# Optimization experiments

Measured on AMD Instinct MI355X. Metric: run time of the kernel, lower is better.

Reference implementation:

```python
import jax, jax.numpy as jnp
import numpy as np
import math

S_DIM = 512
Z_DIM = 64
B, L = 64, 512
NUM_HEADS = 4
HEAD_DIM = S_DIM // NUM_HEADS
N_AA = 20


def _layer_norm(x, eps=1e-5):
    mu = jnp.mean(x, axis=-1, keepdims=True)
    var = jnp.var(x, axis=-1, keepdims=True)
    return (x - mu) * jax.lax.rsqrt(var + eps)


def setup_inputs() -> dict:
    key = jax.random.key(0)
    ks = jax.random.split(key, 16)
    scale = 0.02
    d = {
        's': jax.random.normal(ks[0], (B, L, S_DIM), jnp.float32),
        'z': jax.random.normal(ks[1], (B, L, Z_DIM), jnp.float32),
        'wq': jax.random.normal(ks[2], (S_DIM, S_DIM), jnp.float32) * scale,
        'bq': jnp.zeros((S_DIM,), jnp.float32),
        'wk': jax.random.normal(ks[3], (S_DIM, S_DIM), jnp.float32) * scale,
        'bk': jnp.zeros((S_DIM,), jnp.float32),
        'wv': jax.random.normal(ks[4], (S_DIM, S_DIM), jnp.float32) * scale,
        'bv': jnp.zeros((S_DIM,), jnp.float32),
        'wo': jax.random.normal(ks[5], (S_DIM, S_DIM), jnp.float32) * scale,
        'bo': jnp.zeros((S_DIM,), jnp.float32),
        'wp': jax.random.normal(ks[6], (S_DIM, N_AA), jnp.float32) * scale,
        'bp': jnp.zeros((N_AA,), jnp.float32),
        'pos_bias': jax.random.normal(ks[7], (512,), jnp.float32) * 0.3,
        'entropy_weight': jnp.ones((1,), jnp.float32) * 0.1,
        'ln_g': jnp.ones((S_DIM,), jnp.float32),
        'ln_b': jnp.zeros((S_DIM,), jnp.float32),
        'w1': jax.random.normal(ks[8], (S_DIM, 4 * S_DIM), jnp.float32) * scale,
        'b1': jnp.zeros((4 * S_DIM,), jnp.float32),
        'w2': jax.random.normal(ks[9], (4 * S_DIM, S_DIM), jnp.float32) * scale,
        'b2': jnp.zeros((S_DIM,), jnp.float32),
    }
    return d


def reference(s, z, wq, bq, wk, bk, wv, bv, wo, bo, wp, bp, pos_bias,
              entropy_weight, ln_g, ln_b, w1, b1, w2, b2):
    Bc, Lc, D = s.shape
    H, hd = NUM_HEADS, D // NUM_HEADS

    s_ln = _layer_norm(s)  # non-affine F.layer_norm

    # sequence-profile entropy
    logits = s_ln @ wp + bp                      # [B,L,20]
    profile_probs = jax.nn.softmax(logits, axis=-1)
    position_entropy = -jnp.sum(profile_probs * jnp.log(profile_probs + 1e-8), axis=-1)  # [B,L]

    q = (s_ln @ wq + bq).reshape(Bc, Lc, H, hd)
    k = (s_ln @ wk + bk).reshape(Bc, Lc, H, hd)
    v = (s_ln @ wv + bv).reshape(Bc, Lc, H, hd)

    scores = jnp.einsum('blhd,bmhd->bhlm', q, k) / math.sqrt(hd)  # [B,H,L,L]

    # bias injected only at query index 0, using batch-0 entropy (as in torch code)
    entropy_guidance = -position_entropy[0, :Lc] * entropy_weight[0]  # [L]
    total_bias = entropy_guidance + pos_bias[:Lc]                      # [L]
    scores = scores.at[:, :, 0, :].add(total_bias[None, None, :])

    attn_weights = jax.nn.softmax(scores, axis=-1)                     # [B,H,L,L]
    attn_out = jnp.einsum('bhlm,bmhd->blhd', attn_weights, v).reshape(Bc, Lc, D)

    s2 = s + (attn_out @ wo + bo)

    h = _layer_norm(s2) * ln_g + ln_b
    ffn_out = jax.nn.relu(h @ w1 + b1) @ w2 + b2
    s3 = s2 + ffn_out

    return (s3, z, attn_weights[:, 0, :, :], position_entropy, profile_probs)
```

## Files before the change

### kernel.cpp

```cpp
#include <hip/hip_runtime.h>
#include <hip/hip_bf16.h>
#include <math.h>

#define SDIM 512
#define BATCH 64
#define LSEQ 512
#define NHEAD 4
#define HDIM 128
#define NAA 20
#define NROWS (BATCH * LSEQ)
#define LDQKV 1536

typedef __attribute__((ext_vector_type(8))) short short8;
typedef __attribute__((ext_vector_type(4))) float f32x4;

__device__ __forceinline__ unsigned short f2bf(float f) {
    unsigned int x = __float_as_uint(f);
    unsigned int r = (x + 0x7fffu + ((x >> 16) & 1u)) >> 16;
    return (unsigned short)r;
}
__device__ __forceinline__ float bf2f(unsigned short u) {
    return __uint_as_float((unsigned int)u << 16);
}

__device__ __forceinline__ void load16_lds(const void* g, void* lds) {
    __builtin_amdgcn_global_load_lds(
        (const __attribute__((address_space(1))) unsigned int*)g,
        (__attribute__((address_space(3))) unsigned int*)lds, 16, 0, 0);
}

__device__ __forceinline__ void wtrans_dev(
    float (*tile)[33], const float* __restrict__ W,
    unsigned short* __restrict__ Wt, int K, int N, int bx, int by, int t)
{
    const int tx = t & 31, ty = t >> 5;
    const int n0 = bx * 32, k0 = by * 32;
    #pragma unroll
    for (int p = 0; p < 4; p++)
        tile[ty + p * 8][tx] = W[(size_t)(k0 + ty + p * 8) * N + n0 + tx];
    __syncthreads();
    #pragma unroll
    for (int p = 0; p < 4; p++)
        Wt[(size_t)(n0 + ty + p * 8) * K + k0 + tx] = f2bf(tile[tx][ty + p * 8]);
}

__global__ __launch_bounds__(256) void prep_kernel(
    const float* __restrict__ wq, const float* __restrict__ wk,
    const float* __restrict__ wv, const float* __restrict__ wo,
    const float* __restrict__ w1, const float* __restrict__ w2,
    const float* __restrict__ wp,
    const float* __restrict__ bq, const float* __restrict__ bk,
    const float* __restrict__ bv,
    const float* __restrict__ z,
    const float* __restrict__ s,
    unsigned short* __restrict__ wqkvt, unsigned short* __restrict__ wot,
    unsigned short* __restrict__ w1t, unsigned short* __restrict__ w2t,
    unsigned short* __restrict__ wpT,
    float* __restrict__ bqkv, float* __restrict__ zout,
    unsigned short* __restrict__ Xb)
{
    __shared__ float tile[32][33];
    const int id = blockIdx.x;
    const int t  = threadIdx.x;

    if (id < 256)  { wtrans_dev(tile, wq, wqkvt,          512,  512, id & 15,        id >> 4,        t); return; }
    if (id < 512)  { const int i = id - 256;  wtrans_dev(tile, wk, wqkvt + 262144, 512,  512, i & 15, i >> 4, t); return; }
    if (id < 768)  { const int i = id - 512;  wtrans_dev(tile, wv, wqkvt + 524288, 512,  512, i & 15, i >> 4, t); return; }
    if (id < 1024) { const int i = id - 768;  wtrans_dev(tile, wo, wot,            512,  512, i & 15, i >> 4, t); return; }
    if (id < 2048) { const int i = id - 1024; wtrans_dev(tile, w1, w1t,            512, 2048, i & 63, i >> 6, t); return; }
    if (id < 3072) { const int i = id - 2048; wtrans_dev(tile, w2, w2t,           2048,  512, i & 15, i >> 4, t); return; }
    if (id < 3136) {
        const int g = (id - 3072) * 256 + t;
        const int k = g & 511, j = g >> 9;
        float v = (j < NAA) ? wp[(size_t)k * NAA + j] : 0.0f;
        wpT[(size_t)j * 512 + k] = f2bf(v);
        return;
    }
    if (id == 3136) {
        bqkv[t]        = bq[t];       bqkv[t + 256]  = bq[t + 256];
        bqkv[512 + t]  = bk[t];       bqkv[768 + t]  = bk[t + 256];
        bqkv[1024 + t] = bv[t];       bqkv[1280 + t] = bv[t + 256];
        return;
    }
    if (id < 5185) {
        const size_t i = (size_t)(id - 3137) * 256 + t;
        ((float4*)zout)[i] = ((const float4*)z)[i];
        return;
    }
    {
        const int w = t >> 6, l = t & 63;
        const int r = (id - 5185) * 4 + w;
        const float* row = s + (size_t)r * SDIM;
        float4 a = *(const float4*)(row + l * 4);
        float4 b = *(const float4*)(row + 256 + l * 4);
        float x[8] = {a.x, a.y, a.z, a.w, b.x, b.y, b.z, b.w};

        float sum = 0.f, sq = 0.f;
        #pragma unroll
        for (int i = 0; i < 8; i++) { sum += x[i]; sq += x[i] * x[i]; }
        #pragma unroll
        for (int o = 1; o < 64; o <<= 1) {
            sum += __shfl_xor(sum, o);
            sq  += __shfl_xor(sq, o);
        }
        const float mean = sum * (1.0f / SDIM);
        const float var  = sq * (1.0f / SDIM) - mean * mean;
        const float inv  = rsqrtf(var + 1e-5f);

        float y[8];
        #pragma unroll
        for (int i = 0; i < 8; i++) y[i] = (x[i] - mean) * inv;

        unsigned short* orow = Xb + (size_t)r * SDIM;
        uint2 p0, p1;
        p0.x = (unsigned)f2bf(y[0]) | ((unsigned)f2bf(y[1]) << 16);
        p0.y = (unsigned)f2bf(y[2]) | ((unsigned)f2bf(y[3]) << 16);
        p1.x = (unsigned)f2bf(y[4]) | ((unsigned)f2bf(y[5]) << 16);
        p1.y = (unsigned)f2bf(y[6]) | ((unsigned)f2bf(y[7]) << 16);
        *(uint2*)(orow + l * 4)       = p0;
        *(uint2*)(orow + 256 + l * 4) = p1;
    }
}

template<int INMODE, bool AFFINE>
__global__ __launch_bounds__(256) void ln_kernel(
    const void* __restrict__ inp, unsigned short* __restrict__ out,
    const float* __restrict__ gamma, const float* __restrict__ beta)
{
    const int w = threadIdx.x >> 6, l = threadIdx.x & 63;
    const int r = blockIdx.x * 4 + w;

    float x[8];
    if (INMODE == 0) {
        const float* row = (const float*)inp + (size_t)r * SDIM;
        float4 a = *(const float4*)(row + l * 4);
        float4 b = *(const float4*)(row + 256 + l * 4);
        x[0] = a.x; x[1] = a.y; x[2] = a.z; x[3] = a.w;
        x[4] = b.x; x[5] = b.y; x[6] = b.z; x[7] = b.w;
    } else {
        const unsigned short* row = (const unsigned short*)inp + (size_t)r * SDIM;
        uint2 a = *(const uint2*)(row + l * 4);
        uint2 b = *(const uint2*)(row + 256 + l * 4);
        x[0] = bf2f((unsigned short)(a.x & 0xffff)); x[1] = bf2f((unsigned short)(a.x >> 16));
        x[2] = bf2f((unsigned short)(a.y & 0xffff)); x[3] = bf2f((unsigned short)(a.y >> 16));
        x[4] = bf2f((unsigned short)(b.x & 0xffff)); x[5] = bf2f((unsigned short)(b.x >> 16));
        x[6] = bf2f((unsigned short)(b.y & 0xffff)); x[7] = bf2f((unsigned short)(b.y >> 16));
    }

    float sum = 0.f, sq = 0.f;
    #pragma unroll
    for (int i = 0; i < 8; i++) { sum += x[i]; sq += x[i] * x[i]; }
    #pragma unroll
    for (int o = 1; o < 64; o <<= 1) {
        sum += __shfl_xor(sum, o);
        sq  += __shfl_xor(sq, o);
    }
    const float mean = sum * (1.0f / SDIM);
    const float var  = sq * (1.0f / SDIM) - mean * mean;
    const float inv  = rsqrtf(var + 1e-5f);

    float y[8];
    if (AFFINE) {
        float4 g0 = *(const float4*)(gamma + l * 4);
        float4 g1 = *(const float4*)(gamma + 256 + l * 4);
        float4 b0 = *(const float4*)(beta + l * 4);
        float4 b1 = *(const float4*)(beta + 256 + l * 4);
        y[0] = (x[0]-mean)*inv*g0.x + b0.x; y[1] = (x[1]-mean)*inv*g0.y + b0.y;
        y[2] = (x[2]-mean)*inv*g0.z + b0.z; y[3] = (x[3]-mean)*inv*g0.w + b0.w;
        y[4] = (x[4]-mean)*inv*g1.x + b1.x; y[5] = (x[5]-mean)*inv*g1.y + b1.y;
        y[6] = (x[6]-mean)*inv*g1.z + b1.z; y[7] = (x[7]-mean)*inv*g1.w + b1.w;
    } else {
        #pragma unroll
        for (int i = 0; i < 8; i++) y[i] = (x[i] - mean) * inv;
    }

    unsigned short* orow = out + (size_t)r * SDIM;
    uint2 p0, p1;
    p0.x = (unsigned)f2bf(y[0]) | ((unsigned)f2bf(y[1]) << 16);
    p0.y = (unsigned)f2bf(y[2]) | ((unsigned)f2bf(y[3]) << 16);
    p1.x = (unsigned)f2bf(y[4]) | ((unsigned)f2bf(y[5]) << 16);
    p1.y = (unsigned)f2bf(y[6]) | ((unsigned)f2bf(y[7]) << 16);
    *(uint2*)(orow + l * 4)       = p0;
    *(uint2*)(orow + 256 + l * 4) = p1;
}

__global__ __launch_bounds__(256) void profile_kernel(
    const unsigned short* __restrict__ A,
    const unsigned short* __restrict__ wpT,
    const float* __restrict__ bp,
    float* __restrict__ probs,
    float* __restrict__ pe)
{
    __shared__ __align__(16) unsigned short As[128 * 64];

    const int t = threadIdx.x;
    const int w = t >> 6, l = t & 63;
    const int lr = l & 15, lg = l >> 4;
    const int m0 = blockIdx.x * 128;

    f32x4 sacc[2][2];
    #pragma unroll
    for (int m = 0; m < 2; m++)
        #pragma unroll
        for (int n = 0; n < 2; n++)
            sacc[m][n] = (f32x4){0.f, 0.f, 0.f, 0.f};

    const int srow  = l >> 3;
    const int swz16 = ((l & 7) ^ srow) << 4;
    const char* pA[4];
    unsigned ldsoff[4];
    #pragma unroll
    for (int i = 0; i < 4; i++) {
        const int row = (w * 4 + i) * 8 + srow;
        pA[i] = (const char*)A + (size_t)(m0 + row) * 1024 + swz16;
        ldsoff[i] = (unsigned)(w * 4 + i) * 1024;
    }

    const int rsw   = (lr & 7) << 4;
    const int foff0 = (lg * 16) ^ rsw;
    const int foff1 = (64 + lg * 16) ^ rsw;
    int arow[2];
    #pragma unroll
    for (int m = 0; m < 2; m++) arow[m] = (w * 32 + m * 16 + lr) * 128;

    for (int k0 = 0; k0 < 512; k0 += 64) {
        const size_t kb = (size_t)k0 * 2;
        #pragma unroll
        for (int i = 0; i < 4; i++)
            load16_lds(pA[i] + kb, (char*)As + ldsoff[i]);
        __syncthreads();

        short8 af[2], bf[2];
        #pragma unroll
        for (int m = 0; m < 2; m++) af[m] = *(const short8*)((const char*)As + arow[m] + foff0);
        #pragma unroll
        for (int n = 0; n < 2; n++)
            bf[n] = *(const short8*)(wpT + (size_t)(n * 16 + lr) * 512 + k0 + lg * 8);
        #pragma unroll
        for (int m = 0; m < 2; m++)
            #pragma unroll
            for (int n = 0; n < 2; n++)
                sacc[m][n] = __builtin_amdgcn_mfma_f32_16x16x32_bf16(af[m], bf[n], sacc[m][n], 0, 0, 0);

        #pragma unroll
        for (int m = 0; m < 2; m++) af[m] = *(const short8*)((const char*)As + arow[m] + foff1);
        #pragma unroll
        for (int n = 0; n < 2; n++)
            bf[n] = *(const short8*)(wpT + (size_t)(n * 16 + lr) * 512 + k0 + 32 + lg * 8);
        #pragma unroll
        for (int m = 0; m < 2; m++)
            #pragma unroll
            for (int n = 0; n < 2; n++)
                sacc[m][n] = __builtin_amdgcn_mfma_f32_16x16x32_bf16(af[m], bf[n], sacc[m][n], 0, 0, 0);

        __syncthreads();
    }

    const float b0 = bp[lr];
    const float b1 = (lr < 4) ? bp[16 + lr] : 0.0f;
    #pragma unroll
    for (int m = 0; m < 2; m++) {
        #pragma unroll
        for (int j = 0; j < 4; j++) {
            const float v0 = sacc[m][0][j] + b0;
            const float e0 = __expf(v0);
            const float v1 = sacc[m][1][j] + b1;
            const float e1 = (lr < 4) ? __expf(v1) : 0.0f;
            float Sp = e0 + e1;
            float Tp = e0 * v0 + ((lr < 4) ? e1 * v1 : 0.0f);
            #pragma unroll
            for (int o = 1; o < 16; o <<= 1) {
                Sp += __shfl_xor(Sp, o);
                Tp += __shfl_xor(Tp, o);
            }
            const float inv = 1.0f / Sp;
            const int row = m0 + w * 32 + m * 16 + lg * 4 + j;
            probs[(size_t)row * NAA + lr] = e0 * inv;
            if (lr < 4) probs[(size_t)row * NAA + 16 + lr] = e1 * inv;
            if (lr == 0) pe[row] = logf(Sp) - Tp * inv;
        }
    }
}

template<int OMODE, bool BIAS, bool RELU, int RESID>
__global__ __launch_bounds__(512, 2) void mgemm7(
    const unsigned short* __restrict__ A, int lda,
    const unsigned short* __restrict__ Bt, int ldb,
    void* __restrict__ Cv, int ldc,
    const float* __restrict__ bias,
    const void* __restrict__ R, int ldr,
    int K)
{
    __shared__ __align__(16) char lds[131072];

    const int t = threadIdx.x;
    const int w = t >> 6, l = t & 63;
    const int wr = w >> 2, wc = w & 3;
    const int lg = l >> 4, lr = l & 15;

    const int gx   = gridDim.x;
    const int nwg  = gx * gridDim.y;
    const int flat = blockIdx.x + gx * blockIdx.y;
    const int cpx  = nwg >> 3;
    const int logical = (flat & 7) * cpx + (flat >> 3);
    const int m0 = (logical / gx) * 256, n0 = (logical % gx) * 256;

    f32x4 acc[8][4];
    #pragma unroll
    for (int m = 0; m < 8; m++)
        #pragma unroll
        for (int n = 0; n < 4; n++)
            acc[m][n] = (f32x4){0.f, 0.f, 0.f, 0.f};

    const int srow = t >> 3;
    const int sch  = (t & 7) ^ (srow & 7);

    auto stageA = [&](int kt, int d, int h) {
        const char* src = (const char*)A +
            ((size_t)(m0 + h * 128 + srow) * lda + sch * 8) * 2 + (size_t)kt * 128;
        char* dst = lds + d * 65536 + h * 16384 + t * 16;
        load16_lds(src, dst);
        load16_lds(src + (size_t)64 * lda * 2, dst + 8192);
    };
    auto stageB = [&](int kt, int d, int h) {
        const char* src = (const char*)Bt +
            ((size_t)(n0 + h * 128 + srow) * ldb + sch * 8) * 2 + (size_t)kt * 128;
        char* dst = lds + d * 65536 + 32768 + h * 16384 + t * 16;
        load16_lds(src, dst);
        load16_lds(src + (size_t)64 * ldb * 2, dst + 8192);
    };

    int aoff[4], boff[2], sw[2];
    #pragma unroll
    for (int mi = 0; mi < 4; mi++) aoff[mi] = (mi * 32 + wr * 16 + lr) * 128;
    #pragma unroll
    for (int ni = 0; ni < 2; ni++) boff[ni] = (ni * 64 + wc * 16 + lr) * 128;
    #pragma unroll
    for (int ks = 0; ks < 2; ks++) sw[ks] = ((ks * 4 + lg) ^ (lr & 7)) << 4;

    short8 afc[2][4];
    short8 bfc0[2][2];
    short8 bfc1[2][2];

    const int NI = K >> 7;

#define MPHASE(D, MH, NH, LOADA, LOADB, BAR, STAGE_STMT, WAIT_STMT) do {       \
    const char* Abase_ = lds + (D) * 65536 + (MH) * 16384;                     \
    const char* Bbase_ = lds + (D) * 65536 + 32768 + (NH) * 16384;             \
    if (LOADA) {                                                               \
        _Pragma("unroll")                                                      \
        for (int ks_ = 0; ks_ < 2; ks_++)                                      \
            _Pragma("unroll")                                                  \
            for (int mi_ = 0; mi_ < 4; mi_++)                                  \
                afc[ks_][mi_] = *(const short8*)(Abase_ + aoff[mi_] + sw[ks_]);\
    }                                                                          \
    short8 (&bf_)[2][2] = (NH) ? bfc1 : bfc0;                                  \
    if (LOADB) {                                                               \
        _Pragma("unroll")                                                      \
        for (int ks_ = 0; ks_ < 2; ks_++)                                      \
            _Pragma("unroll")                                                  \
            for (int ni_ = 0; ni_ < 2; ni_++)                                  \
                bf_[ks_][ni_] = *(const short8*)(Bbase_ + boff[ni_] + sw[ks_]);\
    }                                                                          \
    STAGE_STMT;                                                                \
    WAIT_STMT;                                                                 \
    if (BAR) {                                                                 \
        __builtin_amdgcn_s_barrier();                                          \
        asm volatile("s_waitcnt lgkmcnt(0)" ::: "memory");                     \
        __builtin_amdgcn_sched_barrier(0);                                     \
    }                                                                          \
    __builtin_amdgcn_s_setprio(1);                                             \
    _Pragma("unroll")                                                          \
    for (int ks_ = 0; ks_ < 2; ks_++)                                          \
        _Pragma("unroll")                                                      \
        for (int mi_ = 0; mi_ < 4; mi_++)                                      \
            _Pragma("unroll")                                                  \
            for (int ni_ = 0; ni_ < 2; ni_++)                                  \
                acc[(MH) * 4 + mi_][(NH) * 2 + ni_] =                          \
                    __builtin_amdgcn_mfma_f32_16x16x32_bf16(                   \
                        afc[ks_][mi_], bf_[ks_][ni_],                          \
                        acc[(MH) * 4 + mi_][(NH) * 2 + ni_], 0, 0, 0);         \
    __builtin_amdgcn_s_setprio(0);                                             \
    asm volatile("" ::: "memory");                                             \
} while (0)

    stageA(0, 0, 0); stageB(0, 0, 0); stageB(0, 0, 1); stageA(0, 0, 1);
    stageA(1, 1, 0); stageB(1, 1, 0);
    asm volatile("s_waitcnt vmcnt(4)" ::: "memory");
    __builtin_amdgcn_s_barrier();
    asm volatile("" ::: "memory");

    for (int it = 0; it < NI; ++it) {
        const bool more = (it + 1 < NI);
        const int T1 = 2 * it + 1, T2 = 2 * it + 2, T3 = 2 * it + 3;

        MPHASE(0, 0, 0, 1, 1, 1, { stageB(T1, 1, 1); }, {});
        MPHASE(0, 0, 1, 0, 1, 1, { stageA(T1, 1, 1); }, {});
        MPHASE(0, 1, 0, 1, 0, 1, { if (more) stageA(T2, 0, 0); }, {});
        MPHASE(0, 1, 1, 0, 0, 0, { if (more) stageB(T2, 0, 0); },
               { if (more) { asm volatile("s_waitcnt vmcnt(4)" ::: "memory"); }
                 else      { asm volatile("s_waitcnt vmcnt(0)" ::: "memory"); } });
        MPHASE(1, 0, 0, 1, 1, 1, { if (more) stageA(T2, 0, 1); }, {});
        MPHASE(1, 0, 1, 0, 1, 1, { if (more) stageB(T2, 0, 1); }, {});
        MPHASE(1, 1, 0, 1, 0, 1, { if (more) stageA(T3, 1, 0); }, {});
        MPHASE(1, 1, 1, 0, 0, 0, { if (more) stageB(T3, 1, 0); },
               { if (more) { asm volatile("s_waitcnt vmcnt(4)" ::: "memory"); } });
    }
#undef MPHASE

    __syncthreads();

    if (OMODE == 1) {
        unsigned short* cs = (unsigned short*)lds;
        #pragma unroll
        for (int nf = 0; nf < 4; nf++) {
            const int lcol = (nf >> 1) * 128 + (nf & 1) * 64 + wc * 16 + lr;
            const int col = n0 + lcol;
            const float bv = BIAS ? bias[col] : 0.0f;
            #pragma unroll
            for (int mf = 0; mf < 8; mf++) {
                const int lrow0 = (mf >> 2) * 128 + (mf & 3) * 32 + wr * 16 + lg * 4;
                #pragma unroll
                for (int j = 0; j < 4; j++) {
                    float v = acc[mf][nf][j] + bv;
                    if (RELU) v = fmaxf(v, 0.f);
                    const size_t grow = (size_t)(m0 + lrow0 + j);
                    if (RESID == 1) v += ((const float*)R)[grow * ldr + col];
                    if (RESID == 2) v += bf2f(((const unsigned short*)R)[grow * ldr + col]);
                    cs[(lrow0 + j) * 256 + lcol] = f2bf(v);
                }
            }
        }
        __syncthreads();
        unsigned short* Cp = (unsigned short*)Cv;
        #pragma unroll
        for (int i = 0; i < 16; i++) {
            const int slot = i * 512 + t;
            const int row = slot >> 5, c16 = slot & 31;
            short8 v = *(const short8*)(cs + row * 256 + c16 * 8);
            *(short8*)(Cp + (size_t)(m0 + row) * ldc + n0 + c16 * 8) = v;
        }
    } else {
        float* cf = (float*)lds;
        #pragma unroll
        for (int h = 0; h < 2; h++) {
            if (h) __syncthreads();
            #pragma unroll
            for (int nf = 0; nf < 4; nf++) {
                const int lcol = (nf >> 1) * 128 + (nf & 1) * 64 + wc * 16 + lr;
                const int col = n0 + lcol;
                const float bv = BIAS ? bias[col] : 0.0f;
                #pragma unroll
                for (int mi = 0; mi < 4; mi++) {
                    const int mf = h * 4 + mi;
                    const int lrow0 = (mf & 3) * 32 + wr * 16 + lg * 4;
                    #pragma unroll
                    for (int j = 0; j < 4; j++) {
                        float v = acc[mf][nf][j] + bv;
                        if (RELU) v = fmaxf(v, 0.f);
                        const size_t grow = (size_t)(m0 + h * 128 + lrow0 + j);
                        if (RESID == 1) v += ((const float*)R)[grow * ldr + col];
                        if (RESID == 2) v += bf2f(((const unsigned short*)R)[grow * ldr + col]);
                        cf[(lrow0 + j) * 256 + lcol] = v;
                    }
                }
            }
            __syncthreads();
            float* Cp = (float*)Cv;
            #pragma unroll
            for (int i = 0; i < 16; i++) {
                const int slot = i * 512 + t;
                const int row = slot >> 6, c4 = slot & 63;
                float4 v = *(const float4*)(cf + row * 256 + c4 * 4);
                *(float4*)(Cp + (size_t)(m0 + h * 128 + row) * ldc + n0 + c4 * 4) = v;
            }
        }
    }
}

__global__ __launch_bounds__(256, 2) void attn_mfma(
    const unsigned short* __restrict__ QKV,
    const float* __restrict__ pe,
    const float* __restrict__ ew,
    const float* __restrict__ pos,
    unsigned short* __restrict__ AOb,
    float* __restrict__ lgout)
{
    const int flat = blockIdx.x + 4 * (blockIdx.y + 4 * blockIdx.z);
    const int logical = ((flat & 7) << 7) + (flat >> 3);
    const int qt = logical & 3;
    const int h  = (logical >> 2) & 3;
    const int b  = logical >> 4;
    const int t  = threadIdx.x;
    const int w  = t >> 6, l = t & 63;
    const int lr = l & 15, lg = l >> 4;
    const int qbase = qt * 128 + w * 32;

    const unsigned short* Qp = QKV;
    const unsigned short* Kp = QKV + 512;
    const unsigned short* Vp = QKV + 1024;

    __shared__ __align__(16) unsigned short Ks[2][8192];
    __shared__ __align__(16) unsigned short Vt[8192];
    __shared__ __align__(16) unsigned short Pl[8192];
    __shared__ float tbs[512];

    {
        const float e0 = ew[0];
        tbs[t]       = -pe[t]       * e0 + pos[t];
        tbs[t + 256] = -pe[t + 256] * e0 + pos[t + 256];
    }

    short8 qf[2][4];
    #pragma unroll
    for (int fc = 0; fc < 2; fc++) {
        const size_t qrow = (size_t)(b * LSEQ + qbase + fc * 16 + lr) * LDQKV + h * HDIM;
        #pragma unroll
        for (int ks = 0; ks < 4; ks++)
            qf[fc][ks] = *(const short8*)(Qp + qrow + ks * 32 + lg * 8);
    }

    f32x4 oacc[2][8];
    #pragma unroll
    for (int m = 0; m < 2; m++)
        #pragma unroll
        for (int n = 0; n < 8; n++)
            oacc[m][n] = (f32x4){0.f, 0.f, 0.f, 0.f};
    float lpart[2] = {0.f, 0.f};

    const float scale = 0.08838834764831845f;
    unsigned short* Plw = Pl + w * 2048;

    auto stageK = [&](int kt, int buf) {
        #pragma unroll
        for (int it = 0; it < 4; it++) {
            const int bi = it * 4 + w;
            const int r  = bi * 4 + lg;
            const int sc = lr ^ (r & 7);
            const char* src = (const char*)Kp +
                (size_t)(b * LSEQ + kt * 64 + r) * (LDQKV * 2) + h * 256 + sc * 16;
            load16_lds(src, (char*)Ks[buf] + bi * 1024);
        }
    };
    const int k0v = (l & 31) * 2;
    const int d0v = w * 32 + (l >> 5) * 16;

    stageK(0, 0);
    short8 vc0, vc1, vc2, vc3, vn0, vn1, vn2, vn3;
    {
        const size_t vrow = (size_t)(b * LSEQ + k0v) * LDQKV + h * HDIM + d0v;
        vc0 = *(const short8*)(Vp + vrow);
        vc1 = *(const short8*)(Vp + vrow + 8);
        vc2 = *(const short8*)(Vp + vrow + LDQKV);
        vc3 = *(const short8*)(Vp + vrow + LDQKV + 8);
    }

    #pragma unroll 2
    for (int kt = 0; kt < 8; ++kt) {
        asm volatile("" ::: "memory");
        __builtin_amdgcn_s_barrier();
        asm volatile("" ::: "memory");

        if (kt < 7) {
            stageK(kt + 1, (kt + 1) & 1);
            const size_t vrow = (size_t)(b * LSEQ + (kt + 1) * 64 + k0v) * LDQKV + h * HDIM + d0v;
            vn0 = *(const short8*)(Vp + vrow);
            vn1 = *(const short8*)(Vp + vrow + 8);
            vn2 = *(const short8*)(Vp + vrow + LDQKV);
            vn3 = *(const short8*)(Vp + vrow + LDQKV + 8);
        }
        asm volatile("" ::: "memory");

        #pragma unroll
        for (int j = 0; j < 16; j++) {
            const int d = d0v + j;
            unsigned short lo = (unsigned short)((j < 8) ? vc0[j] : vc1[j - 8]);
            unsigned short hi = (unsigned short)((j < 8) ? vc2[j] : vc3[j - 8]);
            unsigned int pk = (unsigned)lo | ((unsigned)hi << 16);
            const int addr = d * 128 + ((((k0v >> 3) ^ (d & 7))) << 4) + (k0v & 7) * 2;
            *(unsigned int*)((char*)Vt + addr) = pk;
        }

        if (kt < 7) { asm volatile("s_waitcnt vmcnt(8)" ::: "memory"); }
        else        { asm volatile("s_waitcnt vmcnt(0)" ::: "memory"); }
        asm volatile("s_waitcnt lgkmcnt(0)" ::: "memory");
        __builtin_amdgcn_s_barrier();
        __builtin_amdgcn_sched_barrier(0);

        const unsigned short* Ksb = Ks[kt & 1];

        f32x4 sacc[4][2];
        #pragma unroll
        for (int fm = 0; fm < 4; fm++)
            #pragma unroll
            for (int fc = 0; fc < 2; fc++)
                sacc[fm][fc] = (f32x4){0.f, 0.f, 0.f, 0.f};
        #pragma unroll
        for (int ks = 0; ks < 4; ks++) {
            short8 af[4];
            #pragma unroll
            for (int fm = 0; fm < 4; fm++) {
                const int r2 = fm * 16 + lr;
                af[fm] = *(const short8*)((const char*)Ksb +
                          r2 * 256 + (((ks * 4 + lg) ^ (lr & 7)) << 4));
            }
            #pragma unroll
            for (int fm = 0; fm < 4; fm++)
                #pragma unroll
                for (int fc = 0; fc < 2; fc++)
                    sacc[fm][fc] = __builtin_amdgcn_mfma_f32_16x16x32_bf16(
                        af[fm], qf[fc][ks], sacc[fm][fc], 0, 0, 0);
        }

        #pragma unroll
        for (int fm = 0; fm < 4; fm++) {
            #pragma unroll
            for (int fc = 0; fc < 2; fc++) {
                float p0 = sacc[fm][fc][0] * scale;
                float p1 = sacc[fm][fc][1] * scale;
                float p2 = sacc[fm][fc][2] * scale;
                float p3 = sacc[fm][fc][3] * scale;
                if (qt == 0 && w == 0 && fc == 0 && lr == 0) {
                    const int kb = kt * 64 + fm * 16 + lg * 4;
                    p0 += tbs[kb + 0]; p1 += tbs[kb + 1];
                    p2 += tbs[kb + 2]; p3 += tbs[kb + 3];
                }
                p0 = __expf(p0); p1 = __expf(p1);
                p2 = __expf(p2); p3 = __expf(p3);
                lpart[fc] += (p0 + p1) + (p2 + p3);
                const int rq = fc * 16 + lr;
                const int chunk = fm * 2 + (lg >> 1);
                const int addr = rq * 128 + ((chunk ^ (rq & 7)) << 4) + (lg & 1) * 8;
                unsigned int lo = (unsigned)f2bf(p0) | ((unsigned)f2bf(p1) << 16);
                unsigned int hi = (unsigned)f2bf(p2) | ((unsigned)f2bf(p3) << 16);
                *(uint2*)((char*)Plw + addr) = make_uint2(lo, hi);
            }
        }

        #pragma unroll
        for (int ks2 = 0; ks2 < 2; ks2++) {
            short8 pf[2];
            #pragma unroll
            for (int fm2 = 0; fm2 < 2; fm2++) {
                const int rq2 = fm2 * 16 + lr;
                pf[fm2] = *(const short8*)((const char*)Plw +
                           rq2 * 128 + (((ks2 * 4 + lg) ^ (rq2 & 7)) << 4));
            }
            #pragma unroll
            for (int fn = 0; fn < 8; fn++) {
                const int d = fn * 16 + lr;
                short8 vf = *(const short8*)((const char*)Vt +
                             d * 128 + (((ks2 * 4 + lg) ^ (d & 7)) << 4));
                #pragma unroll
                for (int fm2 = 0; fm2 < 2; fm2++)
                    oacc[fm2][fn] = __builtin_amdgcn_mfma_f32_16x16x32_bf16(
                        pf[fm2], vf, oacc[fm2][fn], 0, 0, 0);
            }
        }

        vc0 = vn0; vc1 = vn1; vc2 = vn2; vc3 = vn3;
    }

    float l0 = lpart[0], l1 = lpart[1];
    l0 += __shfl_xor(l0, 16); l0 += __shfl_xor(l0, 32);
    l1 += __shfl_xor(l1, 16); l1 += __shfl_xor(l1, 32);
    float* lw = (float*)Plw;
    if (lg == 0) { lw[lr] = l0; lw[16 + lr] = l1; }
    if (h == 0 && lg == 0) {
        lgout[b * LSEQ + qbase + lr]      = l0;
        lgout[b * LSEQ + qbase + 16 + lr] = l1;
    }
    __builtin_amdgcn_s_waitcnt(0);

    #pragma unroll
    for (int fm2 = 0; fm2 < 2; fm2++) {
        float linv[4];
        #pragma unroll
        for (int j = 0; j < 4; j++)
            linv[j] = 1.0f / lw[fm2 * 16 + lg * 4 + j];
        #pragma unroll
        for (int fn = 0; fn < 8; fn++) {
            const int d = fn * 16 + lr;
            #pragma unroll
            for (int j = 0; j < 4; j++) {
                const int q = qbase + fm2 * 16 + lg * 4 + j;
                AOb[(size_t)(b * LSEQ + q) * SDIM + h * HDIM + d] =
                    f2bf(oacc[fm2][fn][j] * linv[j]);
            }
        }
    }
}

__global__ __launch_bounds__(256, 2) void sw0_kernel(
    const unsigned short* __restrict__ QKV,
    const float* __restrict__ pe,
    const float* __restrict__ ew,
    const float* __restrict__ pos,
    const float* __restrict__ lsum,
    float* __restrict__ W0)
{
    const int flat = blockIdx.x + 4 * blockIdx.y;
    const int logical = ((flat & 7) << 5) + (flat >> 3);
    const int qt = logical & 3;
    const int b  = logical >> 2;
    const int t  = threadIdx.x;
    const int w  = t >> 6, l = t & 63;
    const int lr = l & 15, lg = l >> 4;
    const int qbase = qt * 128 + w * 32;

    const unsigned short* Qp = QKV;
    const unsigned short* Kp = QKV + 512;

    __shared__ __align__(16) unsigned short Ks[2][8192];
    __shared__ __align__(16) float Sc[4][32][68];
    __shared__ float tbs[512];

    {
        const float e0 = ew[0];
        tbs[t]       = -pe[t]       * e0 + pos[t];
        tbs[t + 256] = -pe[t + 256] * e0 + pos[t + 256];
    }

    short8 qf[2][4];
    #pragma unroll
    for (int fc = 0; fc < 2; fc++) {
        const size_t qrow = (size_t)(b * LSEQ + qbase + fc * 16 + lr) * LDQKV;
        #pragma unroll
        for (int ks = 0; ks < 4; ks++)
            qf[fc][ks] = *(const short8*)(Qp + qrow + ks * 32 + lg * 8);
    }

    float linv[2];
    linv[0] = 1.0f / lsum[b * LSEQ + qbase + lr];
    linv[1] = 1.0f / lsum[b * LSEQ + qbase + 16 + lr];

    const float scale = 0.08838834764831845f;

    auto stageK = [&](int kt, int buf) {
        #pragma unroll
        for (int it = 0; it < 4; it++) {
            const int bi = it * 4 + w;
            const int r  = bi * 4 + lg;
            const int sc = lr ^ (r & 7);
            const char* src = (const char*)Kp +
                (size_t)(b * LSEQ + kt * 64 + r) * (LDQKV * 2) + sc * 16;
            load16_lds(src, (char*)Ks[buf] + bi * 1024);
        }
    };

    stageK(0, 0);

    for (int kt = 0; kt < 8; ++kt) {
        asm volatile("" ::: "memory");
        __builtin_amdgcn_s_barrier();
        asm volatile("" ::: "memory");

        if (kt < 7) stageK(kt + 1, (kt + 1) & 1);

        if (kt < 7) { asm volatile("s_waitcnt vmcnt(4)" ::: "memory"); }
        else        { asm volatile("s_waitcnt vmcnt(0)" ::: "memory"); }
        __builtin_amdgcn_s_barrier();
        __builtin_amdgcn_sched_barrier(0);

        const unsigned short* Ksb = Ks[kt & 1];

        f32x4 sacc[4][2];
        #pragma unroll
        for (int fm = 0; fm < 4; fm++)
            #pragma unroll
            for (int fc = 0; fc < 2; fc++)
                sacc[fm][fc] = (f32x4){0.f, 0.f, 0.f, 0.f};
        #pragma unroll
        for (int ks = 0; ks < 4; ks++) {
            short8 af[4];
            #pragma unroll
            for (int fm = 0; fm < 4; fm++) {
                const int r2 = fm * 16 + lr;
                af[fm] = *(const short8*)((const char*)Ksb +
                          r2 * 256 + (((ks * 4 + lg) ^ (lr & 7)) << 4));
            }
            #pragma unroll
            for (int fm = 0; fm < 4; fm++)
                #pragma unroll
                for (int fc = 0; fc < 2; fc++)
                    sacc[fm][fc] = __builtin_amdgcn_mfma_f32_16x16x32_bf16(
                        af[fm], qf[fc][ks], sacc[fm][fc], 0, 0, 0);
        }

        #pragma unroll
        for (int fm = 0; fm < 4; fm++) {
            #pragma unroll
            for (int fc = 0; fc < 2; fc++) {
                float p0 = sacc[fm][fc][0] * scale;
                float p1 = sacc[fm][fc][1] * scale;
                float p2 = sacc[fm][fc][2] * scale;
                float p3 = sacc[fm][fc][3] * scale;
                if (qt == 0 && w == 0 && fc == 0 && lr == 0) {
                    const int kb = kt * 64 + fm * 16 + lg * 4;
                    p0 += tbs[kb + 0]; p1 += tbs[kb + 1];
                    p2 += tbs[kb + 2]; p3 += tbs[kb + 3];
                }
                p0 = __expf(p0) * linv[fc]; p1 = __expf(p1) * linv[fc];
                p2 = __expf(p2) * linv[fc]; p3 = __expf(p3) * linv[fc];
                *(float4*)&Sc[w][fc * 16 + lr][fm * 16 + lg * 4] =
                    make_float4(p0, p1, p2, p3);
            }
        }

        #pragma unroll
        for (int i = 0; i < 8; i++) {
            const int row = i * 4 + lg;
            float4 v = *(const float4*)&Sc[w][row][lr * 4];
            *(float4*)(W0 + (size_t)(b * LSEQ + qbase + row) * LSEQ +
                       kt * 64 + lr * 4) = v;
        }
    }
}

extern "C" void kernel_launch(void* const* d_in, const int* in_sizes, int n_in,
                              void* d_out, int out_size, void* d_ws, size_t ws_size,
                              hipStream_t stream)
{
    const float* s   = (const float*)d_in[0];
    const float* z   = (const float*)d_in[1];
    const float* wq  = (const float*)d_in[2];
    const float* bq  = (const float*)d_in[3];
    const float* wk  = (const float*)d_in[4];
    const float* bk  = (const float*)d_in[5];
    const float* wv  = (const float*)d_in[6];
    const float* bv  = (const float*)d_in[7];
    const float* wo  = (const float*)d_in[8];
    const float* bo  = (const float*)d_in[9];
    const float* wp  = (const float*)d_in[10];
    const float* bp  = (const float*)d_in[11];
    const float* pos = (const float*)d_in[12];
    const float* ew  = (const float*)d_in[13];
    const float* lng = (const float*)d_in[14];
    const float* lnb = (const float*)d_in[15];
    const float* w1  = (const float*)d_in[16];
    const float* b1  = (const float*)d_in[17];
    const float* w2  = (const float*)d_in[18];
    const float* b2  = (const float*)d_in[19];

    float* out = (float*)d_out;
    const size_t oz  = (size_t)NROWS * SDIM;
    const size_t ow  = oz + (size_t)NROWS * 64;
    const size_t ope = ow + (size_t)NROWS * LSEQ;
    const size_t opr = ope + (size_t)NROWS;

    char* wsb = (char*)d_ws;
    unsigned short* QKV = (unsigned short*)(wsb);
    unsigned short* F   = (unsigned short*)(wsb);
    unsigned short* Xb  = (unsigned short*)(wsb + 100663296);
    unsigned short* s2b = (unsigned short*)(wsb + 134217728);
    unsigned short* hb  = (unsigned short*)(wsb + 167772160);
    unsigned short* wqkvt = (unsigned short*)(wsb + 234881024);
    unsigned short* wot = wqkvt + 786432;
    unsigned short* w1t = wqkvt + 1048576;
    unsigned short* w2t = wqkvt + 2097152;
    unsigned short* wpT = wqkvt + 3145728;
    float* bqkv = (float*)(wsb + 234881024 + 6324224);
    float* lgv  = bqkv + 2048;

    prep_kernel<<<13377, 256, 0, stream>>>(
        wq, wk, wv, wo, w1, w2, wp, bq, bk, bv, z, s,
        wqkvt, wot, w1t, w2t, wpT, bqkv, out + oz, Xb);

    profile_kernel<<<256, 256, 0, stream>>>(Xb, wpT, bp, out + opr, out + ope);

    mgemm7<1, true, false, 0><<<dim3(6, 128), 512, 0, stream>>>(
        Xb, 512, wqkvt, 512, QKV, LDQKV, bqkv, nullptr, 0, 512);

    attn_mfma<<<dim3(4, NHEAD, BATCH), 256, 0, stream>>>(
        QKV, out + ope, ew, pos, Xb, lgv);

    sw0_kernel<<<dim3(4, BATCH), 256, 0, stream>>>(
        QKV, out + ope, ew, pos, lgv, out + ow);

    mgemm7<1, true, false, 1><<<dim3(2, 128), 512, 0, stream>>>(
        Xb, 512, wot, 512, s2b, 512, bo, s, 512, 512);

    ln_kernel<1, true><<<NROWS / 4, 256, 0, stream>>>(s2b, hb, lng, lnb);

    mgemm7<1, true, true, 0><<<dim3(8, 128), 512, 0, stream>>>(
        hb, 512, w1t, 512, F, 2048, b1, nullptr, 0, 512);

    mgemm7<0, true, false, 2><<<dim3(2, 128), 512, 0, stream>>>(
        F, 2048, w2t, 2048, out, 512, b2, s2b, 512, 2048);
}
```

Before: 399.8 us.

## Fuse head-0 attention-weight output into attention kernel, drop sw0 launch

Removes the separate sw0 kernel that recomputed head-0 QK^T scores and normalized probabilities. Head-0 attention blocks now reuse their already-loaded Q fragments, K staging and row sums to recompute scores and write normalized weights, using the merged V/P shared buffer as scratch. This saves a kernel launch, a redundant Q load and the row-sum round trip through global memory. The cost is that head-0 blocks run noticeably longer than the other heads, which can cause load imbalance in the attention grid.

```diff
diff --git a/kernel.cpp b/kernel.cpp
--- a/kernel.cpp
+++ b/kernel.cpp
@@ -484,7 +484,7 @@
     const float* __restrict__ ew,
     const float* __restrict__ pos,
     unsigned short* __restrict__ AOb,
-    float* __restrict__ lgout)
+    float* __restrict__ W0)
 {
     const int flat = blockIdx.x + 4 * (blockIdx.y + 4 * blockIdx.z);
     const int logical = ((flat & 7) << 7) + (flat >> 3);
@@ -501,9 +501,10 @@
     const unsigned short* Vp = QKV + 1024;
 
     __shared__ __align__(16) unsigned short Ks[2][8192];
-    __shared__ __align__(16) unsigned short Vt[8192];
-    __shared__ __align__(16) unsigned short Pl[8192];
+    __shared__ __align__(16) unsigned short VtPl[16384];
     __shared__ float tbs[512];
+    unsigned short* Vt = VtPl;
+    unsigned short* Pl = VtPl + 8192;
 
     {
         const float e0 = ew[0];
@@ -666,11 +667,11 @@
     l1 += __shfl_xor(l1, 16); l1 += __shfl_xor(l1, 32);
     float* lw = (float*)Plw;
     if (lg == 0) { lw[lr] = l0; lw[16 + lr] = l1; }
-    if (h == 0 && lg == 0) {
-        lgout[b * LSEQ + qbase + lr]      = l0;
-        lgout[b * LSEQ + qbase + 16 + lr] = l1;
-    }
     __builtin_amdgcn_s_waitcnt(0);
+
+    float linvp[2];
+    linvp[0] = 1.0f / lw[lr];
+    linvp[1] = 1.0f / lw[16 + lr];
 
     #pragma unroll
     for (int fm2 = 0; fm2 < 2; fm2++) {
@@ -689,130 +690,77 @@
             }
         }
     }
-}
-
-__global__ __launch_bounds__(256, 2) void sw0_kernel(
-    const unsigned short* __restrict__ QKV,
-    const float* __restrict__ pe,
-    const float* __restrict__ ew,
-    const float* __restrict__ pos,
-    const float* __restrict__ lsum,
-    float* __restrict__ W0)
-{
-    const int flat = blockIdx.x + 4 * blockIdx.y;
-    const int logical = ((flat & 7) << 5) + (flat >> 3);
-    const int qt = logical & 3;
-    const int b  = logical >> 2;
-    const int t  = threadIdx.x;
-    const int w  = t >> 6, l = t & 63;
-    const int lr = l & 15, lg = l >> 4;
-    const int qbase = qt * 128 + w * 32;
-
-    const unsigned short* Qp = QKV;
-    const unsigned short* Kp = QKV + 512;
-
-    __shared__ __align__(16) unsigned short Ks[2][8192];
-    __shared__ __align__(16) float Sc[4][32][68];
-    __shared__ float tbs[512];
-
-    {
-        const float e0 = ew[0];
-        tbs[t]       = -pe[t]       * e0 + pos[t];
-        tbs[t + 256] = -pe[t + 256] * e0 + pos[t + 256];
-    }
-
-    short8 qf[2][4];
-    #pragma unroll
-    for (int fc = 0; fc < 2; fc++) {
-        const size_t qrow = (size_t)(b * LSEQ + qbase + fc * 16 + lr) * LDQKV;
-        #pragma unroll
-        for (int ks = 0; ks < 4; ks++)
-            qf[fc][ks] = *(const short8*)(Qp + qrow + ks * 32 + lg * 8);
-    }
-
-    float linv[2];
-    linv[0] = 1.0f / lsum[b * LSEQ + qbase + lr];
-    linv[1] = 1.0f / lsum[b * LSEQ + qbase + 16 + lr];
-
-    const float scale = 0.08838834764831845f;
-
-    auto stageK = [&](int kt, int buf) {
-        #pragma unroll
-        for (int it = 0; it < 4; it++) {
-            const int bi = it * 4 + w;
-            const int r  = bi * 4 + lg;
-            const int sc = lr ^ (r & 7);
-            const char* src = (const char*)Kp +
-                (size_t)(b * LSEQ + kt * 64 + r) * (LDQKV * 2) + sc * 16;
-            load16_lds(src, (char*)Ks[buf] + bi * 1024);
-        }
-    };
-
-    stageK(0, 0);
-
-    for (int kt = 0; kt < 8; ++kt) {
-        asm volatile("" ::: "memory");
-        __builtin_amdgcn_s_barrier();
-        asm volatile("" ::: "memory");
-
-        if (kt < 7) stageK(kt + 1, (kt + 1) & 1);
-
-        if (kt < 7) { asm volatile("s_waitcnt vmcnt(4)" ::: "memory"); }
-        else        { asm volatile("s_waitcnt vmcnt(0)" ::: "memory"); }
-        __builtin_amdgcn_s_barrier();
-        __builtin_amdgcn_sched_barrier(0);
-
-        const unsigned short* Ksb = Ks[kt & 1];
-
-        f32x4 sacc[4][2];
-        #pragma unroll
-        for (int fm = 0; fm < 4; fm++)
-            #pragma unroll
-            for (int fc = 0; fc < 2; fc++)
-                sacc[fm][fc] = (f32x4){0.f, 0.f, 0.f, 0.f};
-        #pragma unroll
-        for (int ks = 0; ks < 4; ks++) {
-            short8 af[4];
-            #pragma unroll
-            for (int fm = 0; fm < 4; fm++) {
-                const int r2 = fm * 16 + lr;
-                af[fm] = *(const short8*)((const char*)Ksb +
-                          r2 * 256 + (((ks * 4 + lg) ^ (lr & 7)) << 4));
-            }
+
+    if (h == 0) {
+        float* Sc = (float*)VtPl;
+        float* Scw = Sc + w * 2048;
+
+        stageK(0, 0);
+
+        for (int kt = 0; kt < 8; ++kt) {
+            asm volatile("" ::: "memory");
+            __builtin_amdgcn_s_barrier();
+            asm volatile("" ::: "memory");
+
+            if (kt < 7) stageK(kt + 1, (kt + 1) & 1);
+
+            if (kt < 7) { asm volatile("s_waitcnt vmcnt(4)" ::: "memory"); }
+            else        { asm volatile("s_waitcnt vmcnt(0)" ::: "memory"); }
+            __builtin_amdgcn_s_barrier();
+            __builtin_amdgcn_sched_barrier(0);
+
+            const unsigned short* Ksb = Ks[kt & 1];
+
+            f32x4 sacc[4][2];
             #pragma unroll
             for (int fm = 0; fm < 4; fm++)
                 #pragma unroll
                 for (int fc = 0; fc < 2; fc++)
-                    sacc[fm][fc] = __builtin_amdgcn_mfma_f32_16x16x32_bf16(
-                        af[fm], qf[fc][ks], sacc[fm][fc], 0, 0, 0);
-        }
-
-        #pragma unroll
-        for (int fm = 0; fm < 4; fm++) {
-            #pragma unroll
-            for (int fc = 0; fc < 2; fc++) {
-                float p0 = sacc[fm][fc][0] * scale;
-                float p1 = sacc[fm][fc][1] * scale;
-                float p2 = sacc[fm][fc][2] * scale;
-                float p3 = sacc[fm][fc][3] * scale;
-                if (qt == 0 && w == 0 && fc == 0 && lr == 0) {
-                    const int kb = kt * 64 + fm * 16 + lg * 4;
-                    p0 += tbs[kb + 0]; p1 += tbs[kb + 1];
-                    p2 += tbs[kb + 2]; p3 += tbs[kb + 3];
+                    sacc[fm][fc] = (f32x4){0.f, 0.f, 0.f, 0.f};
+            #pragma unroll
+            for (int ks = 0; ks < 4; ks++) {
+                short8 af[4];
+                #pragma unroll
+                for (int fm = 0; fm < 4; fm++) {
+                    const int r2 = fm * 16 + lr;
+                    af[fm] = *(const short8*)((const char*)Ksb +
+                              r2 * 256 + (((ks * 4 + lg) ^ (lr & 7)) << 4));
                 }
-                p0 = __expf(p0) * linv[fc]; p1 = __expf(p1) * linv[fc];
-                p2 = __expf(p2) * linv[fc]; p3 = __expf(p3) * linv[fc];
-                *(float4*)&Sc[w][fc * 16 + lr][fm * 16 + lg * 4] =
-                    make_float4(p0, p1, p2, p3);
-            }
-        }
-
-        #pragma unroll
-        for (int i = 0; i < 8; i++) {
-            const int row = i * 4 + lg;
-            float4 v = *(const float4*)&Sc[w][row][lr * 4];
-            *(float4*)(W0 + (size_t)(b * LSEQ + qbase + row) * LSEQ +
-                       kt * 64 + lr * 4) = v;
+                #pragma unroll
+                for (int fm = 0; fm < 4; fm++)
+                    #pragma unroll
+                    for (int fc = 0; fc < 2; fc++)
+                        sacc[fm][fc] = __builtin_amdgcn_mfma_f32_16x16x32_bf16(
+                            af[fm], qf[fc][ks], sacc[fm][fc], 0, 0, 0);
+            }
+
+            #pragma unroll
+            for (int fm = 0; fm < 4; fm++) {
+                #pragma unroll
+                for (int fc = 0; fc < 2; fc++) {
+                    float p0 = sacc[fm][fc][0] * scale;
+                    float p1 = sacc[fm][fc][1] * scale;
+                    float p2 = sacc[fm][fc][2] * scale;
+                    float p3 = sacc[fm][fc][3] * scale;
+                    if (qt == 0 && w == 0 && fc == 0 && lr == 0) {
+                        const int kb = kt * 64 + fm * 16 + lg * 4;
+                        p0 += tbs[kb + 0]; p1 += tbs[kb + 1];
+                        p2 += tbs[kb + 2]; p3 += tbs[kb + 3];
+                    }
+                    p0 = __expf(p0) * linvp[fc]; p1 = __expf(p1) * linvp[fc];
+                    p2 = __expf(p2) * linvp[fc]; p3 = __expf(p3) * linvp[fc];
+                    *(float4*)&Scw[(fc * 16 + lr) * 64 + fm * 16 + lg * 4] =
+                        make_float4(p0, p1, p2, p3);
+                }
+            }
+
+            #pragma unroll
+            for (int i = 0; i < 8; i++) {
+                const int row = i * 4 + lg;
+                float4 v = *(const float4*)&Scw[row * 64 + lr * 4];
+                *(float4*)(W0 + (size_t)(b * LSEQ + qbase + row) * LSEQ +
+                           kt * 64 + lr * 4) = v;
+            }
         }
     }
 }
@@ -860,7 +808,6 @@
     unsigned short* w2t = wqkvt + 2097152;
     unsigned short* wpT = wqkvt + 3145728;
     float* bqkv = (float*)(wsb + 234881024 + 6324224);
-    float* lgv  = bqkv + 2048;
 
     prep_kernel<<<13377, 256, 0, stream>>>(
         wq, wk, wv, wo, w1, w2, wp, bq, bk, bv, z, s,
@@ -872,10 +819,7 @@
         Xb, 512, wqkvt, 512, QKV, LDQKV, bqkv, nullptr, 0, 512);
 
     attn_mfma<<<dim3(4, NHEAD, BATCH), 256, 0, stream>>>(
-        QKV, out + ope, ew, pos, Xb, lgv);
-
-    sw0_kernel<<<dim3(4, BATCH), 256, 0, stream>>>(
-        QKV, out + ope, ew, pos, lgv, out + ow);
+        QKV, out + ope, ew, pos, Xb, out + ow);
 
     mgemm7<1, true, false, 1><<<dim3(2, 128), 512, 0, stream>>>(
         Xb, 512, wot, 512, s2b, 512, bo, s, 512, 512);
```

Result: no change. 405.0 us (+1.3%).
